# Kernel optimization log

Measured on AMD Instinct MI355X. Metric: run time of the kernel, lower is better.

The kernel has to match this reference:

```python
import jax, jax.numpy as jnp
import numpy as np

B, T, C = 2, 2048, 1024
NH = 16
HD = C // NH

def build_alibi_bias(n_head, max_len):
    slopes = jnp.arange(1, n_head + 1, dtype=jnp.float32) / n_head  # [nh]
    ar = jnp.arange(max_len, dtype=jnp.float32)
    # bias[h, i, j] = slopes[h] * (j - i)
    return slopes[:, None, None] * (ar[None, None, :] - ar[None, :, None])

def setup_inputs() -> dict:
    key = jax.random.key(0)
    ks = jax.random.split(key, 7)
    s = 0.02
    return {
        "x": jax.random.normal(ks[0], (B, T, C), dtype=jnp.float32),
        "q_w": jax.random.normal(ks[1], (C, C), dtype=jnp.float32) * s,   # [in, out]
        "q_b": jnp.zeros((C,), dtype=jnp.float32),
        "kv_w": jax.random.normal(ks[2], (C, 2 * C), dtype=jnp.float32) * s,
        "kv_b": jnp.zeros((2 * C,), dtype=jnp.float32),
        "o_w": jax.random.normal(ks[3], (C, C), dtype=jnp.float32) * s,
        "o_b": jnp.zeros((C,), dtype=jnp.float32),
    }

def reference(x, q_w, q_b, kv_w, kv_b, o_w, o_b):
    Bx, Tx, Cx = x.shape
    q = (x @ q_w + q_b).reshape(Bx, Tx, NH, HD).transpose(0, 2, 1, 3)      # [B,nh,T,hd]
    kv = (x @ kv_w + kv_b).reshape(Bx, Tx, 2, NH, HD).transpose(2, 0, 3, 1, 4)
    k, v = kv[0], kv[1]                                                     # [B,nh,T,hd]
    att = jnp.einsum("bhqd,bhkd->bhqk", q, k) * (1.0 / np.sqrt(HD))        # [B,nh,T,T]
    att = att + build_alibi_bias(NH, Tx)[None]                              # ALiBi bias
    causal = jnp.tril(jnp.ones((Tx, Tx), dtype=bool))
    att = jnp.where(causal[None, None], att, -jnp.inf)
    att = jax.nn.softmax(att, axis=-1)
    y = jnp.einsum("bhqk,bhkd->bhqd", att, v)                               # [B,nh,T,hd]
    y = y.transpose(0, 2, 1, 3).reshape(Bx, Tx, Cx)
    return y @ o_w + o_b
```

## Files before the change

kernel.cpp:

```cpp
#include <hip/hip_runtime.h>
#include <hip/hip_bf16.h>

#define NB 2
#define NT 2048
#define NC 1024
#define NHD 16
#define HDD 64
#define LOG2E 1.4426950408889634f

typedef __attribute__((ext_vector_type(8))) short short8;
typedef __attribute__((ext_vector_type(4))) float f32x4;
typedef __attribute__((ext_vector_type(16))) float f32x16;

__device__ __forceinline__ ushort f2bf(float f) {
    union { float f; unsigned u; } v; v.f = f;
    unsigned u = v.u;
    unsigned r = (u + 0x7FFFu + ((u >> 16) & 1u)) >> 16;
    return (ushort)r;
}

__device__ __forceinline__ unsigned pkbf(float a, float b) {
    __hip_bfloat162 t = __float22bfloat162_rn(float2{a, b});
    unsigned u; __builtin_memcpy(&u, &t, 4); return u;
}

__device__ __forceinline__ void gload16(const ushort* g, ushort* l) {
    __builtin_amdgcn_global_load_lds((const __attribute__((address_space(1))) void*)g,
                                     (__attribute__((address_space(3))) void*)l, 16, 0, 0);
}

__global__ __launch_bounds__(256)
void cvtx(const float* __restrict__ src, ushort* __restrict__ dst, int n)
{
    int i = (blockIdx.x * 256 + threadIdx.x) * 8;
    if (i >= n) return;
    float4 a = *(const float4*)(src + i);
    float4 b = *(const float4*)(src + i + 4);
    short8 o;
    o[0] = (short)f2bf(a.x); o[1] = (short)f2bf(a.y);
    o[2] = (short)f2bf(a.z); o[3] = (short)f2bf(a.w);
    o[4] = (short)f2bf(b.x); o[5] = (short)f2bf(b.y);
    o[6] = (short)f2bf(b.z); o[7] = (short)f2bf(b.w);
    *(short8*)(dst + i) = o;
}

__global__ __launch_bounds__(256)
void tcvt(const float* __restrict__ src, ushort* __restrict__ dst, int Kd, int Nd)
{
    __shared__ ushort tile[64][68];
    const int tid = threadIdx.x;
    const int kb = blockIdx.x * 64, nb = blockIdx.y * 64;
    const int r = tid >> 2, c = (tid & 3) * 16;
    const float* sp = src + (size_t)(kb + r) * Nd + nb + c;
#pragma unroll
    for (int i = 0; i < 16; i += 4) {
        float4 v = *(const float4*)(sp + i);
        tile[r][c + i + 0] = f2bf(v.x);
        tile[r][c + i + 1] = f2bf(v.y);
        tile[r][c + i + 2] = f2bf(v.z);
        tile[r][c + i + 3] = f2bf(v.w);
    }
    __syncthreads();
    ushort* dp = dst + (size_t)(nb + r) * Kd + kb + c;
#pragma unroll
    for (int i = 0; i < 16; i += 8) {
        short8 o;
#pragma unroll
        for (int j = 0; j < 8; j++) o[j] = (short)tile[c + i + j][r];
        *(short8*)(dp + i) = o;
    }
}

__global__ __launch_bounds__(256)
void vtr(const ushort* __restrict__ src, ushort* __restrict__ dst)
{
    __shared__ ushort tile[64][66];
    const int tid = threadIdx.x;
    const int bh = blockIdx.y;
    const int t0 = blockIdx.x * 64;
    const int r = tid >> 2, c = (tid & 3) * 16;
    const ushort* sp = src + ((size_t)bh * NT + t0 + r) * HDD + c;
    *(short8*)&tile[r][c]     = *(const short8*)sp;
    *(short8*)&tile[r][c + 8] = *(const short8*)(sp + 8);
    __syncthreads();
    ushort* dp = dst + ((size_t)bh * HDD + r) * NT + t0 + c;
    short8 o0, o1;
#pragma unroll
    for (int j = 0; j < 8; j++) { o0[j] = (short)tile[c + j][r]; o1[j] = (short)tile[c + 8 + j][r]; }
    *(short8*)dp = o0;
    *(short8*)(dp + 8) = o1;
}

template<int MODE>
__global__ __launch_bounds__(256)
void gemm128(const ushort* __restrict__ A, const ushort* __restrict__ Bt,
             const float* __restrict__ bias0, const float* __restrict__ bias1,
             ushort* __restrict__ Qo, ushort* __restrict__ Ko, ushort* __restrict__ Vo,
             float* __restrict__ Fo, int Kdim)
{
    __shared__ ushort Al[128 * 32];
    __shared__ ushort Bl[128 * 32];
    const int tid = threadIdx.x;
    const int lane = tid & 63, w = tid >> 6;
    const int wr = (w >> 1) * 64, wc = (w & 1) * 64;
    const int lg = lane >> 4, lc = lane & 15;
    const int bm = blockIdx.x * 128, bn = blockIdx.y * 128;

    f32x4 acc[4][4] = {};

    const int srow = lane >> 2, scol = (lane & 3) * 8;

    for (int k0 = 0; k0 < Kdim; k0 += 32) {
        __syncthreads();
#pragma unroll
        for (int c = 0; c < 2; c++) {
            int seg = w * 2 + c;
            int row = seg * 16 + srow;
            gload16(A  + (size_t)(bm + row) * Kdim + k0 + scol, &Al[seg * 512]);
            gload16(Bt + (size_t)(bn + row) * Kdim + k0 + scol, &Bl[seg * 512]);
        }
        __syncthreads();
        short8 af[4], bfv[4];
#pragma unroll
        for (int mt = 0; mt < 4; mt++) af[mt] = *(const short8*)&Al[(wr + mt*16 + lc) * 32 + lg*8];
#pragma unroll
        for (int nt = 0; nt < 4; nt++) bfv[nt] = *(const short8*)&Bl[(wc + nt*16 + lc) * 32 + lg*8];
#pragma unroll
        for (int mt = 0; mt < 4; mt++)
#pragma unroll
            for (int nt = 0; nt < 4; nt++)
                acc[mt][nt] = __builtin_amdgcn_mfma_f32_16x16x32_bf16(af[mt], bfv[nt], acc[mt][nt], 0, 0, 0);
    }

#pragma unroll
    for (int mt = 0; mt < 4; mt++) {
#pragma unroll
        for (int nt = 0; nt < 4; nt++) {
#pragma unroll
            for (int rr = 0; rr < 4; rr++) {
                int m = bm + wr + mt*16 + lg*4 + rr;
                int n = bn + wc + nt*16 + lc;
                float v = acc[mt][nt][rr];
                if (MODE == 0) {
                    int b = m >> 11, t = m & 2047;
                    if (n < NC) {
                        float q = (v + bias0[n]) * (0.125f * LOG2E);
                        int hh = n >> 6, d = n & 63;
                        Qo[(((size_t)b*NHD + hh)*NT + t)*HDD + d] = f2bf(q);
                    } else {
                        int j = n - NC;
                        float val = v + bias1[j];
                        int s = j >> 10;
                        int jj = j & 1023;
                        int hh = jj >> 6, d = jj & 63;
                        ushort* dst = s ? Vo : Ko;
                        dst[(((size_t)b*NHD + hh)*NT + t)*HDD + d] = f2bf(val);
                    }
                } else {
                    Fo[(size_t)m * NC + n] = v + bias0[n];
                }
            }
        }
    }
}

__global__ __launch_bounds__(256, 3)
void attn_fwd(const ushort* __restrict__ Q, const ushort* __restrict__ K,
              const ushort* __restrict__ Vt, ushort* __restrict__ Y)
{
    __shared__ ushort sb[2 * 64 * 72];
    ushort* Kl = sb;
    ushort* Vl = sb + 64 * 72;

    const int tid = threadIdx.x;
    const int lane = tid & 63, w = tid >> 6;
    const int lo5 = lane & 31, hi = lane >> 5;
    const int qt = 15 - (int)(blockIdx.x >> 5);
    const int bh = blockIdx.x & 31;
    const int b = bh >> 4, h = bh & 15;

    const ushort* Qp = Q + (size_t)bh * NT * HDD;
    const ushort* Kp = K + (size_t)bh * NT * HDD;
    const ushort* Vp = Vt + (size_t)bh * HDD * NT;

    const int bq0 = qt * 128;
    const int q0 = bq0 + w * 32;
    const int qlane = q0 + lo5;

    const float slope2 = (float)(h + 1) * (LOG2E / (float)NHD);

    short8 qf[4];
    {
        const ushort* qr = Qp + (size_t)qlane * HDD + 8 * hi;
#pragma unroll
        for (int kk = 0; kk < 4; kk++) qf[kk] = *(const short8*)(qr + kk * 16);
    }

    float bb[16];
#pragma unroll
    for (int r = 0; r < 16; r++) {
        int roff = (r & 3) + 8 * (r >> 2) + 4 * hi;
        bb[r] = slope2 * ((float)roff - (float)qlane);
    }

    float m_s = -1e30f, l_s = 0.f;
    f32x16 accO[2] = {};

    const int ntile = 2 * qt + 2;
    const int sr = tid >> 2, sd = (tid & 3) * 16;

    short8 pk0, pk1, pv0, pv1;
    {
        const ushort* kp = Kp + (size_t)sr * HDD + sd;
        pk0 = *(const short8*)kp;
        pk1 = *(const short8*)(kp + 8);
        const ushort* vp = Vp + (size_t)sr * NT + sd;
        pv0 = *(const short8*)vp;
        pv1 = *(const short8*)(vp + 8);
    }

    for (int t = 0; t < ntile; t++) {
        const int kv0 = t * 64;
        __syncthreads();
        *(short8*)&Kl[sr * 72 + sd]     = pk0;
        *(short8*)&Kl[sr * 72 + sd + 8] = pk1;
        *(short8*)&Vl[sr * 72 + sd]     = pv0;
        *(short8*)&Vl[sr * 72 + sd + 8] = pv1;
        __syncthreads();

        if (t + 1 < ntile) {
            const int kv1 = kv0 + 64;
            const ushort* kp = Kp + (size_t)(kv1 + sr) * HDD + sd;
            pk0 = *(const short8*)kp;
            pk1 = *(const short8*)(kp + 8);
            const ushort* vp = Vp + (size_t)sr * NT + kv1 + sd;
            pv0 = *(const short8*)vp;
            pv1 = *(const short8*)(vp + 8);
        }

#pragma unroll
        for (int sub = 0; sub < 2; sub++) {
            const int kv0s = kv0 + sub * 32;
            if (kv0s > q0 + 31) continue;

            f32x16 S = {};
#pragma unroll
            for (int kk = 0; kk < 4; kk++) {
                short8 kf = *(const short8*)&Kl[(sub * 32 + lo5) * 72 + kk * 16 + 8 * hi];
                S = __builtin_amdgcn_mfma_f32_32x32x16_bf16(kf, qf[kk], S, 0, 0, 0);
            }

            const float sk = slope2 * (float)kv0s;
            float mloc = m_s - sk;

            if (kv0s + 31 > q0) {
#pragma unroll
                for (int r = 0; r < 16; r++) {
                    int kvr = kv0s + (r & 3) + 8 * (r >> 2) + 4 * hi;
                    S[r] = (kvr > qlane) ? -1e30f : (S[r] + bb[r]);
                }
            } else {
#pragma unroll
                for (int r = 0; r < 16; r++) S[r] = S[r] + bb[r];
            }

            float rmax = S[0];
#pragma unroll
            for (int r = 1; r < 16; r++) rmax = fmaxf(rmax, S[r]);
            rmax = fmaxf(rmax, __shfl_xor(rmax, 32));

            if (__any(rmax - mloc > 8.0f)) {
                float mn = fmaxf(mloc, rmax);
                float sc = __builtin_amdgcn_exp2f(mloc - mn);
                mloc = mn;
                l_s *= sc;
#pragma unroll
                for (int dt = 0; dt < 2; dt++)
#pragma unroll
                    for (int r = 0; r < 16; r++) accO[dt][r] *= sc;
            }
            m_s = mloc + sk;

            float p[16], sum = 0.f;
#pragma unroll
            for (int r = 0; r < 16; r++) {
                p[r] = __builtin_amdgcn_exp2f(S[r] - mloc);
                sum += p[r];
            }
            sum += __shfl_xor(sum, 32);
            l_s += sum;

            unsigned pw[8], px[8];
#pragma unroll
            for (int i = 0; i < 8; i++) pw[i] = pkbf(p[2 * i], p[2 * i + 1]);
#pragma unroll
            for (int i = 0; i < 8; i++) px[i] = __shfl_xor(pw[i], 32);
            union { unsigned u[4]; short8 s; } fa0, fa1;
            fa0.u[0] = hi ? px[2] : pw[0];
            fa0.u[1] = hi ? px[3] : pw[1];
            fa0.u[2] = hi ? pw[2] : px[0];
            fa0.u[3] = hi ? pw[3] : px[1];
            fa1.u[0] = hi ? px[6] : pw[4];
            fa1.u[1] = hi ? px[7] : pw[5];
            fa1.u[2] = hi ? pw[6] : px[4];
            fa1.u[3] = hi ? pw[7] : px[5];

#pragma unroll
            for (int dt = 0; dt < 2; dt++) {
                short8 vf0 = *(const short8*)&Vl[(dt * 32 + lo5) * 72 + sub * 32 + 8 * hi];
                short8 vf1 = *(const short8*)&Vl[(dt * 32 + lo5) * 72 + sub * 32 + 16 + 8 * hi];
                accO[dt] = __builtin_amdgcn_mfma_f32_32x32x16_bf16(vf0, fa0.s, accO[dt], 0, 0, 0);
                accO[dt] = __builtin_amdgcn_mfma_f32_32x32x16_bf16(vf1, fa1.s, accO[dt], 0, 0, 0);
            }
        }
    }

    const float invl = __builtin_amdgcn_rcpf(l_s);
    __syncthreads();
    ushort* myO = sb + w * 32 * 72;
#pragma unroll
    for (int dt = 0; dt < 2; dt++)
#pragma unroll
        for (int r = 0; r < 16; r++) {
            int d = dt * 32 + (r & 3) + 8 * (r >> 2) + 4 * hi;
            myO[lo5 * 72 + d] = f2bf(accO[dt][r] * invl);
        }
    __syncthreads();
    const int orow = lane >> 1, ocol = (lane & 1) * 32;
    const int qg = q0 + orow;
    ushort* yp = Y + ((size_t)b * NT + qg) * NC + h * HDD + ocol;
#pragma unroll
    for (int c = 0; c < 4; c++)
        *(short8*)(yp + c * 8) = *(const short8*)&myO[orow * 72 + ocol + c * 8];
}

extern "C" void kernel_launch(void* const* d_in, const int* in_sizes, int n_in,
                              void* d_out, int out_size, void* d_ws, size_t ws_size,
                              hipStream_t stream)
{
    const float* x    = (const float*)d_in[0];
    const float* q_w  = (const float*)d_in[1];
    const float* q_b  = (const float*)d_in[2];
    const float* kv_w = (const float*)d_in[3];
    const float* kv_b = (const float*)d_in[4];
    const float* o_w  = (const float*)d_in[5];
    const float* o_b  = (const float*)d_in[6];
    float* out = (float*)d_out;

    char* ws = (char*)d_ws;
    ushort* xb    = (ushort*)(ws);
    ushort* wqkvT = (ushort*)(ws + 8388608);
    ushort* woT   = (ushort*)(ws + 14680064);
    ushort* Qs    = (ushort*)(ws + 16777216);
    ushort* Ks    = (ushort*)(ws + 25165824);
    ushort* Vs    = (ushort*)(ws + 33554432);
    ushort* Ys    = (ushort*)(ws + 41943040);
    ushort* VsT   = xb;

    cvtx<<<2048, 256, 0, stream>>>(x, xb, NB*NT*NC);
    tcvt<<<dim3(16,16), 256, 0, stream>>>(q_w, wqkvT, 1024, 1024);
    tcvt<<<dim3(16,32), 256, 0, stream>>>(kv_w, wqkvT + 1024*1024, 1024, 2048);
    tcvt<<<dim3(16,16), 256, 0, stream>>>(o_w, woT, 1024, 1024);
    gemm128<0><<<dim3(32,24), 256, 0, stream>>>(xb, wqkvT, q_b, kv_b, Qs, Ks, Vs, nullptr, 1024);
    vtr<<<dim3(32,32), 256, 0, stream>>>(Vs, VsT);
    attn_fwd<<<512, 256, 0, stream>>>(Qs, Ks, VsT, Ys);
    gemm128<1><<<dim3(32,8), 256, 0, stream>>>(Ys, woT, o_b, nullptr, nullptr, nullptr, nullptr, out, 1024);
}
```

Before: 150.2 us.

## Fuse prep conversions into one kernel; shrink attention blocks and double-buffer K/V

Merges the x conversion and three weight transpose-convert launches into a single prep kernel, which cuts launch overhead. The attention kernel now runs 128-thread blocks (two waves, 64 query rows) across 1024 blocks instead of 256-thread blocks over 512. K/V tiles are double-buffered in LDS, so one of the two barriers per tile goes away, and each thread stages 64 bytes per tile. This gives finer causal load balancing and less sync, at the cost of twice the LDS per block and reloading K/V once per 64-row query chunk instead of once per 128 rows.

```diff
diff --git a/kernel.cpp b/kernel.cpp
--- a/kernel.cpp
+++ b/kernel.cpp
@@ -29,27 +29,11 @@
                                      (__attribute__((address_space(3))) void*)l, 16, 0, 0);
 }
 
-__global__ __launch_bounds__(256)
-void cvtx(const float* __restrict__ src, ushort* __restrict__ dst, int n)
-{
-    int i = (blockIdx.x * 256 + threadIdx.x) * 8;
-    if (i >= n) return;
-    float4 a = *(const float4*)(src + i);
-    float4 b = *(const float4*)(src + i + 4);
-    short8 o;
-    o[0] = (short)f2bf(a.x); o[1] = (short)f2bf(a.y);
-    o[2] = (short)f2bf(a.z); o[3] = (short)f2bf(a.w);
-    o[4] = (short)f2bf(b.x); o[5] = (short)f2bf(b.y);
-    o[6] = (short)f2bf(b.z); o[7] = (short)f2bf(b.w);
-    *(short8*)(dst + i) = o;
-}
-
-__global__ __launch_bounds__(256)
-void tcvt(const float* __restrict__ src, ushort* __restrict__ dst, int Kd, int Nd)
+__device__ __forceinline__ void tcvt_tile(const float* __restrict__ src, ushort* __restrict__ dst,
+                                          int Kd, int Nd, int kb, int nb)
 {
     __shared__ ushort tile[64][68];
     const int tid = threadIdx.x;
-    const int kb = blockIdx.x * 64, nb = blockIdx.y * 64;
     const int r = tid >> 2, c = (tid & 3) * 16;
     const float* sp = src + (size_t)(kb + r) * Nd + nb + c;
 #pragma unroll
@@ -68,6 +52,34 @@
 #pragma unroll
         for (int j = 0; j < 8; j++) o[j] = (short)tile[c + i + j][r];
         *(short8*)(dp + i) = o;
+    }
+}
+
+__global__ __launch_bounds__(256)
+void prep(const float* __restrict__ x, const float* __restrict__ q_w,
+          const float* __restrict__ kv_w, const float* __restrict__ o_w,
+          ushort* __restrict__ xb, ushort* __restrict__ wqkvT, ushort* __restrict__ woT)
+{
+    const int bid = blockIdx.x;
+    if (bid < 2048) {
+        int i = (bid * 256 + threadIdx.x) * 8;
+        float4 a = *(const float4*)(x + i);
+        float4 b = *(const float4*)(x + i + 4);
+        short8 o;
+        o[0] = (short)f2bf(a.x); o[1] = (short)f2bf(a.y);
+        o[2] = (short)f2bf(a.z); o[3] = (short)f2bf(a.w);
+        o[4] = (short)f2bf(b.x); o[5] = (short)f2bf(b.y);
+        o[6] = (short)f2bf(b.z); o[7] = (short)f2bf(b.w);
+        *(short8*)(xb + i) = o;
+    } else if (bid < 2304) {
+        int r = bid - 2048;
+        tcvt_tile(q_w, wqkvT, 1024, 1024, (r & 15) * 64, (r >> 4) * 64);
+    } else if (bid < 2816) {
+        int r = bid - 2304;
+        tcvt_tile(kv_w, wqkvT + 1024 * 1024, 1024, 2048, (r & 15) * 64, (r >> 4) * 64);
+    } else {
+        int r = bid - 2816;
+        tcvt_tile(o_w, woT, 1024, 1024, (r & 15) * 64, (r >> 4) * 64);
     }
 }
 
@@ -164,18 +176,15 @@
     }
 }
 
-__global__ __launch_bounds__(256, 3)
+__global__ __launch_bounds__(128, 4)
 void attn_fwd(const ushort* __restrict__ Q, const ushort* __restrict__ K,
               const ushort* __restrict__ Vt, ushort* __restrict__ Y)
 {
-    __shared__ ushort sb[2 * 64 * 72];
-    ushort* Kl = sb;
-    ushort* Vl = sb + 64 * 72;
-
+    __shared__ ushort sb[4 * 64 * 72];
     const int tid = threadIdx.x;
     const int lane = tid & 63, w = tid >> 6;
     const int lo5 = lane & 31, hi = lane >> 5;
-    const int qt = 15 - (int)(blockIdx.x >> 5);
+    const int qc = 31 - (int)(blockIdx.x >> 5);
     const int bh = blockIdx.x & 31;
     const int b = bh >> 4, h = bh & 15;
 
@@ -183,8 +192,7 @@
     const ushort* Kp = K + (size_t)bh * NT * HDD;
     const ushort* Vp = Vt + (size_t)bh * HDD * NT;
 
-    const int bq0 = qt * 128;
-    const int q0 = bq0 + w * 32;
+    const int q0 = qc * 64 + w * 32;
     const int qlane = q0 + lo5;
 
     const float slope2 = (float)(h + 1) * (LOG2E / (float)NHD);
@@ -206,36 +214,40 @@
     float m_s = -1e30f, l_s = 0.f;
     f32x16 accO[2] = {};
 
-    const int ntile = 2 * qt + 2;
-    const int sr = tid >> 2, sd = (tid & 3) * 16;
-
-    short8 pk0, pk1, pv0, pv1;
+    const int ntile = qc + 1;
+    const int sr = tid >> 1, sd = (tid & 1) * 32;
+
+    short8 pk[4], pv[4];
     {
         const ushort* kp = Kp + (size_t)sr * HDD + sd;
-        pk0 = *(const short8*)kp;
-        pk1 = *(const short8*)(kp + 8);
         const ushort* vp = Vp + (size_t)sr * NT + sd;
-        pv0 = *(const short8*)vp;
-        pv1 = *(const short8*)(vp + 8);
+#pragma unroll
+        for (int i = 0; i < 4; i++) {
+            pk[i] = *(const short8*)(kp + i * 8);
+            pv[i] = *(const short8*)(vp + i * 8);
+        }
     }
 
     for (int t = 0; t < ntile; t++) {
         const int kv0 = t * 64;
-        __syncthreads();
-        *(short8*)&Kl[sr * 72 + sd]     = pk0;
-        *(short8*)&Kl[sr * 72 + sd + 8] = pk1;
-        *(short8*)&Vl[sr * 72 + sd]     = pv0;
-        *(short8*)&Vl[sr * 72 + sd + 8] = pv1;
+        ushort* Kl = sb + (t & 1) * 2 * 64 * 72;
+        ushort* Vl = Kl + 64 * 72;
+#pragma unroll
+        for (int i = 0; i < 4; i++) {
+            *(short8*)&Kl[sr * 72 + sd + i * 8] = pk[i];
+            *(short8*)&Vl[sr * 72 + sd + i * 8] = pv[i];
+        }
         __syncthreads();
 
         if (t + 1 < ntile) {
             const int kv1 = kv0 + 64;
             const ushort* kp = Kp + (size_t)(kv1 + sr) * HDD + sd;
-            pk0 = *(const short8*)kp;
-            pk1 = *(const short8*)(kp + 8);
             const ushort* vp = Vp + (size_t)sr * NT + kv1 + sd;
-            pv0 = *(const short8*)vp;
-            pv1 = *(const short8*)(vp + 8);
+#pragma unroll
+            for (int i = 0; i < 4; i++) {
+                pk[i] = *(const short8*)(kp + i * 8);
+                pv[i] = *(const short8*)(vp + i * 8);
+            }
         }
 
 #pragma unroll
@@ -357,12 +369,9 @@
     ushort* Ys    = (ushort*)(ws + 41943040);
     ushort* VsT   = xb;
 
-    cvtx<<<2048, 256, 0, stream>>>(x, xb, NB*NT*NC);
-    tcvt<<<dim3(16,16), 256, 0, stream>>>(q_w, wqkvT, 1024, 1024);
-    tcvt<<<dim3(16,32), 256, 0, stream>>>(kv_w, wqkvT + 1024*1024, 1024, 2048);
-    tcvt<<<dim3(16,16), 256, 0, stream>>>(o_w, woT, 1024, 1024);
+    prep<<<3072, 256, 0, stream>>>(x, q_w, kv_w, o_w, xb, wqkvT, woT);
     gemm128<0><<<dim3(32,24), 256, 0, stream>>>(xb, wqkvT, q_b, kv_b, Qs, Ks, Vs, nullptr, 1024);
     vtr<<<dim3(32,32), 256, 0, stream>>>(Vs, VsT);
-    attn_fwd<<<512, 256, 0, stream>>>(Qs, Ks, VsT, Ys);
+    attn_fwd<<<1024, 128, 0, stream>>>(Qs, Ks, VsT, Ys);
     gemm128<1><<<dim3(32,8), 256, 0, stream>>>(Ys, woT, o_b, nullptr, nullptr, nullptr, nullptr, out, 1024);
 }
```

After: 159.2 us. 1.06x slower.
